# Optimization experiments

Hardware: AMD Instinct MI355X
Metric: run time of the kernel (lower is better)

Reference implementation:

```python
import jax, jax.numpy as jnp
import numpy as np

IN_FEATURES = 128
OUT_FEATURES = 64
NUM_HEADS = 4
NEGATIVE_SLOPE = 0.2


def setup_inputs() -> dict:
    key = jax.random.key(0)
    k1, k2, k3, k4 = jax.random.split(key, 4)
    B, N = 2, 4096
    inputs = jax.random.normal(k1, (B, N, IN_FEATURES), dtype=jnp.float32)
    # glorot-style scales
    s_w = (6.0 / (IN_FEATURES + OUT_FEATURES * NUM_HEADS)) ** 0.5
    s_a = (6.0 / (OUT_FEATURES + 1)) ** 0.5
    W = jax.random.uniform(k2, (IN_FEATURES, OUT_FEATURES * NUM_HEADS), jnp.float32, -s_w, s_w)
    a_src = jax.random.uniform(k3, (NUM_HEADS, OUT_FEATURES, 1), jnp.float32, -s_a, s_a)
    a_dst = jax.random.uniform(k4, (NUM_HEADS, OUT_FEATURES, 1), jnp.float32, -s_a, s_a)
    bias = jnp.zeros((OUT_FEATURES * NUM_HEADS,), dtype=jnp.float32)
    return {"inputs": inputs, "W": W, "a_src": a_src, "a_dst": a_dst, "bias": bias}


def reference(inputs, W, a_src, a_dst, bias):
    B, N, _ = inputs.shape
    H, D = a_src.shape[0], a_src.shape[1]
    # project and split heads: [B, H, N, D]
    h = jnp.matmul(inputs, W).reshape(B, N, H, D).transpose(0, 2, 1, 3)
    # additive attention scalars per node per head
    e_src = jnp.einsum('bhnd,hd->bhn', h, a_src[..., 0])  # a_src^T (W h_i)
    e_dst = jnp.einsum('bhnd,hd->bhn', h, a_dst[..., 0])  # a_dst^T (W h_j)
    # e[b,h,i,j] = e_src[b,h,i] + e_dst[b,h,j]  (matches e_src + e_dst^T in TF code)
    e = e_src[:, :, :, None] + e_dst[:, :, None, :]
    e = jnp.where(e > 0, e, NEGATIVE_SLOPE * e)  # leaky_relu
    alpha = jax.nn.softmax(e, axis=-1)  # softmax over neighbors j
    # weighted sum of values: [B, H, N, D]
    out = jnp.einsum('bhij,bhjd->bhid', alpha, h)
    out = out.transpose(0, 2, 1, 3).reshape(B, N, H * D)  # concat heads
    out = out + bias
    return jax.nn.elu(out)
```

## Files before the change

### kernel.cpp

```cpp
#include <hip/hip_runtime.h>
#include <hip/hip_fp16.h>
#include <math.h>

#define NH 4
#define DD 64
#define NF 256
#define KF 128
#define NN 4096
#define NB 2
#define NG 8
#define CH 64
#define NCH 64
#define PSUB 16
#define SSUB 8
#define TE 65

typedef _Float16 h8_t __attribute__((ext_vector_type(8)));
typedef float f4_t __attribute__((ext_vector_type(4)));

__global__ __launch_bounds__(256) void k_gemm(const float* __restrict__ X,
                                              const float* __restrict__ W,
                                              const float* __restrict__ a_src,
                                              const float* __restrict__ a_dst,
                                              __half* __restrict__ Hout,
                                              float* __restrict__ s_arr,
                                              float* __restrict__ d_arr) {
  __shared__ float As[64][132];
  __shared__ _Float16 WT[64][136];
  const int bm = blockIdx.x;
  const int bn = blockIdx.y;
  const int tid = threadIdx.x;

  for (int i = tid; i < 64 * 32; i += 256) {
    int r = i >> 5, c4 = i & 31;
    float4 v = *(const float4*)(X + ((size_t)(bm * 64 + r)) * KF + c4 * 4);
    *(float4*)&As[r][c4 * 4] = v;
  }
  for (int i = tid; i < 64 * 128; i += 256) {
    int k = i >> 6, c = i & 63;
    WT[c][k] = (_Float16)W[(size_t)k * NF + bn * 64 + c];
  }
  __syncthreads();

  const int lane = tid & 63, w = tid >> 6;
  const int l15 = lane & 15, lq = lane >> 4;

  f4_t acc[4] = {f4_t{0.f,0.f,0.f,0.f}, f4_t{0.f,0.f,0.f,0.f},
                 f4_t{0.f,0.f,0.f,0.f}, f4_t{0.f,0.f,0.f,0.f}};

  #pragma unroll
  for (int kk = 0; kk < 4; ++kk) {
    const int koff = kk * 32 + lq * 8;
    h8_t a;
    {
      const float* ap = &As[w * 16 + l15][koff];
      float4 x0 = *(const float4*)ap;
      float4 x1 = *(const float4*)(ap + 4);
      a[0] = (_Float16)x0.x; a[1] = (_Float16)x0.y;
      a[2] = (_Float16)x0.z; a[3] = (_Float16)x0.w;
      a[4] = (_Float16)x1.x; a[5] = (_Float16)x1.y;
      a[6] = (_Float16)x1.z; a[7] = (_Float16)x1.w;
    }
    #pragma unroll
    for (int t = 0; t < 4; ++t) {
      h8_t b = *(const h8_t*)&WT[t * 16 + l15][koff];
      acc[t] = __builtin_amdgcn_mfma_f32_16x16x32_f16(a, b, acc[t], 0, 0, 0);
    }
  }

  float asv[4], adv[4];
  #pragma unroll
  for (int t = 0; t < 4; ++t) {
    asv[t] = a_src[bn * 64 + t * 16 + l15];
    adv[t] = a_dst[bn * 64 + t * 16 + l15];
  }
  #pragma unroll
  for (int j = 0; j < 4; ++j) {
    const int grow = bm * 64 + w * 16 + lq * 4 + j;
    float ps = 0.f, pd = 0.f;
    #pragma unroll
    for (int t = 0; t < 4; ++t) {
      float hv = acc[t][j];
      Hout[(size_t)grow * NF + bn * 64 + t * 16 + l15] = __float2half(hv);
      ps += hv * asv[t];
      pd += hv * adv[t];
    }
    #pragma unroll
    for (int off = 1; off < 16; off <<= 1) {
      ps += __shfl_xor(ps, off);
      pd += __shfl_xor(pd, off);
    }
    if (l15 == 0) {
      int b = grow >> 12, n = grow & (NN - 1);
      int g = b * NH + bn;
      s_arr[g * NN + n] = ps;
      d_arr[g * NN + n] = pd;
    }
  }
}

__global__ __launch_bounds__(512) void k_sort(const float* __restrict__ d_arr,
                                              const float* __restrict__ s_arr,
                                              float* __restrict__ dsort, int* __restrict__ dperm,
                                              float* __restrict__ tsort, int* __restrict__ tperm) {
  __shared__ unsigned skey[8][512];
  __shared__ float vals[NN];
  const int bid = blockIdx.x;
  const bool isT = bid >= NG;
  const int g = isT ? bid - NG : bid;
  const float* src = isT ? s_arr : d_arr;
  float* okey = isT ? tsort : dsort;
  int* operm = isT ? tperm : dperm;
  const int tid = threadIdx.x;

  unsigned kk[8];
  {
    float4 v0 = *(const float4*)(src + g * NN + 8 * tid);
    float4 v1 = *(const float4*)(src + g * NN + 8 * tid + 4);
    float f[8] = {v0.x, v0.y, v0.z, v0.w, v1.x, v1.y, v1.z, v1.w};
    #pragma unroll
    for (int r = 0; r < 8; ++r) {
      float fv = isT ? -f[r] : f[r];
      vals[8 * tid + r] = fv;
      unsigned u = __float_as_uint(fv);
      u = (u & 0x80000000u) ? ~u : (u | 0x80000000u);
      kk[r] = (u & 0xFFFFF000u) | (unsigned)(8 * tid + r);
    }
  }

  #define CEU(a, b, asc)                                           \
    do { unsigned ka = kk[a], kb = kk[b];                          \
      unsigned mn = ka < kb ? ka : kb, mx = ka < kb ? kb : ka;     \
      kk[a] = (asc) ? mn : mx; kk[b] = (asc) ? mx : mn; } while (0)

  CEU(0, 1, true); CEU(2, 3, false); CEU(4, 5, true); CEU(6, 7, false);
  CEU(0, 2, true); CEU(1, 3, true); CEU(4, 6, false); CEU(5, 7, false);
  CEU(0, 1, true); CEU(2, 3, true); CEU(4, 5, false); CEU(6, 7, false);

  #pragma unroll
  for (int k = 8; k <= NN; k <<= 1) {
    const bool asc = (tid & (k >> 3)) == 0;
    #pragma unroll
    for (int j = k >> 1; j > 0; j >>= 1) {
      if (j >= 512) {
        const int tdist = j >> 3;
        #pragma unroll
        for (int r = 0; r < 8; ++r) skey[r][tid] = kk[r];
        __syncthreads();
        const bool keepMin = ((tid & tdist) == 0) == asc;
        #pragma unroll
        for (int r = 0; r < 8; ++r) {
          unsigned pk = skey[r][tid ^ tdist];
          unsigned mn = kk[r] < pk ? kk[r] : pk;
          unsigned mx = kk[r] < pk ? pk : kk[r];
          kk[r] = keepMin ? mn : mx;
        }
        __syncthreads();
      } else if (j >= 8) {
        const int dist = j >> 3;
        const bool keepMin = ((tid & dist) == 0) == asc;
        #pragma unroll
        for (int r = 0; r < 8; ++r) {
          unsigned pk = (unsigned)__shfl_xor((int)kk[r], dist);
          unsigned mn = kk[r] < pk ? kk[r] : pk;
          unsigned mx = kk[r] < pk ? pk : kk[r];
          kk[r] = keepMin ? mn : mx;
        }
      } else if (j == 4) {
        CEU(0, 4, asc); CEU(1, 5, asc); CEU(2, 6, asc); CEU(3, 7, asc);
      } else if (j == 2) {
        CEU(0, 2, asc); CEU(1, 3, asc); CEU(4, 6, asc); CEU(5, 7, asc);
      } else {
        CEU(0, 1, asc); CEU(2, 3, asc); CEU(4, 5, asc); CEU(6, 7, asc);
      }
    }
  }
  #undef CEU

  float ov[8]; int op[8];
  #pragma unroll
  for (int r = 0; r < 8; ++r) {
    int idx = (int)(kk[r] & 0xFFFu);
    ov[r] = vals[idx];
    op[r] = idx;
  }
  *(float4*)(okey + g * NN + 8 * tid)     = make_float4(ov[0], ov[1], ov[2], ov[3]);
  *(float4*)(okey + g * NN + 8 * tid + 4) = make_float4(ov[4], ov[5], ov[6], ov[7]);
  *(int4*)(operm + g * NN + 8 * tid)      = make_int4(op[0], op[1], op[2], op[3]);
  *(int4*)(operm + g * NN + 8 * tid + 4)  = make_int4(op[4], op[5], op[6], op[7]);
}

__global__ __launch_bounds__(256) void k_part(const __half* __restrict__ Hmat,
                                              const float* __restrict__ dsort,
                                              const int* __restrict__ dperm,
                                              float* __restrict__ chunkP, float* __restrict__ chunkS,
                                              float* __restrict__ chunkPw, float* __restrict__ chunkSw) {
  __shared__ float subP[4][64], subS[4][64];
  __shared__ float subPw[4], subSw[4];
  const int ch = blockIdx.x;
  const int g = blockIdx.y;
  const int b = g >> 2, h = g & 3;
  const int c = threadIdx.x & 63;
  const int w = threadIdx.x >> 6;
  const int gNN = g * NN;
  const size_t bNN = (size_t)b * NN;
  const int h64 = h * 64;
  const float dmax = dsort[gNN + NN - 1];
  const int kw0 = ch * CH + w * PSUB;

  int j16[PSUB]; float d16[PSUB], hv16[PSUB];
  #pragma unroll
  for (int l = 0; l < PSUB; ++l) j16[l] = dperm[gNN + kw0 + l];
  #pragma unroll
  for (int l = 0; l < PSUB; ++l) d16[l] = dsort[gNN + kw0 + l];
  #pragma unroll
  for (int l = 0; l < PSUB; ++l) hv16[l] = __half2float(Hmat[(bNN + j16[l]) * NF + h64 + c]);

  float pa = 0.f, sa = 0.f, pw = 0.f, sw = 0.f;
  #pragma unroll
  for (int l = 0; l < PSUB; ++l) {
    float wp = __expf(0.2f * (d16[l] - dmax));
    float w2 = wp * wp;
    float ws = w2 * w2 * wp;
    pa += wp * hv16[l]; sa += ws * hv16[l]; pw += wp; sw += ws;
  }
  subP[w][c] = pa; subS[w][c] = sa;
  if (c == 0) { subPw[w] = pw; subSw[w] = sw; }
  __syncthreads();

  if (w == 0) {
    float tp = subP[0][c] + subP[1][c] + subP[2][c] + subP[3][c];
    float ts = subS[0][c] + subS[1][c] + subS[2][c] + subS[3][c];
    chunkP[(g * NCH + ch) * 64 + c] = tp;
    chunkS[(g * NCH + ch) * 64 + c] = ts;
    if (c == 0) {
      chunkPw[g * NCH + ch] = subPw[0] + subPw[1] + subPw[2] + subPw[3];
      chunkSw[g * NCH + ch] = subSw[0] + subSw[1] + subSw[2] + subSw[3];
    }
  }
}

__global__ __launch_bounds__(512) void k_serve(const __half* __restrict__ Hmat,
                                               const float* __restrict__ dsort,
                                               const int* __restrict__ dperm,
                                               const float* __restrict__ tsort,
                                               const int* __restrict__ tperm,
                                               const float* __restrict__ chunkP, const float* __restrict__ chunkS,
                                               const float* __restrict__ chunkPw, const float* __restrict__ chunkSw,
                                               const float* __restrict__ bias,
                                               float* __restrict__ out) {
  __shared__ float PPloc[TE][64], PSloc[TE][64];
  __shared__ float ppwLoc[TE], pswLoc[TE];
  __shared__ float subP[8][64], subS[8][64], sall[8][64];
  __shared__ float subPw[8], subSw[8];

  const int ch = blockIdx.x & (NCH - 1);
  const int g = blockIdx.x >> 6;
  const int b = g >> 2, h = g & 3;
  const int c = threadIdx.x & 63;
  const int w = threadIdx.x >> 6;
  const int gNN = g * NN;
  const size_t bNN = (size_t)b * NN;
  const int h64 = h * 64;
  const float dmax = dsort[gNN + NN - 1];
  const int kw0 = ch * CH + w * SSUB;

  int j8[SSUB]; float d8[SSUB], hv8[SSUB];
  #pragma unroll
  for (int l = 0; l < SSUB; ++l) j8[l] = dperm[gNN + kw0 + l];
  #pragma unroll
  for (int l = 0; l < SSUB; ++l) d8[l] = dsort[gNN + kw0 + l];
  #pragma unroll
  for (int l = 0; l < SSUB; ++l) hv8[l] = __half2float(Hmat[(bNN + j8[l]) * NF + h64 + c]);

  float ppv[SSUB], psv[SSUB], ppw[SSUB], psw[SSUB];
  {
    float ap = 0.f, as = 0.f, aw = 0.f, aswv = 0.f;
    #pragma unroll
    for (int l = 0; l < SSUB; ++l) {
      float wp = __expf(0.2f * (d8[l] - dmax));
      float w2 = wp * wp;
      float ws = w2 * w2 * wp;
      ap += wp * hv8[l]; as += ws * hv8[l]; aw += wp; aswv += ws;
      ppv[l] = ap; psv[l] = as; ppw[l] = aw; psw[l] = aswv;
    }
    subP[w][c] = ap; subS[w][c] = as;
    if (c == 0) { subPw[w] = aw; subSw[w] = aswv; }
  }
  __syncthreads();

  {
    float oP = 0.f, oS = 0.f, oPw = 0.f, oSw = 0.f;
    #pragma unroll
    for (int t = 0; t < 8; ++t) {
      if (t < w) { oP += subP[t][c]; oS += subS[t][c]; oPw += subPw[t]; oSw += subSw[t]; }
    }
    #pragma unroll
    for (int l = 0; l < SSUB; ++l) {
      PPloc[w * SSUB + 1 + l][c] = ppv[l] + oP;
      PSloc[w * SSUB + 1 + l][c] = psv[l] + oS;
    }
    if (c == 0) {
      #pragma unroll
      for (int l = 0; l < SSUB; ++l) {
        ppwLoc[w * SSUB + 1 + l] = ppw[l] + oPw;
        pswLoc[w * SSUB + 1 + l] = psw[l] + oSw;
      }
    }
    if (w == 0) {
      PPloc[0][c] = 0.f; PSloc[0][c] = 0.f;
      if (c == 0) { ppwLoc[0] = 0.f; pswLoc[0] = 0.f; }
    }
  }
  __syncthreads();

  {
    float pp = 0.f, sp = 0.f, sa = 0.f;
    for (int t = w; t < ch; t += 8) pp += chunkP[(g * NCH + t) * 64 + c];
    for (int t = w; t < NCH; t += 8) {
      float v = chunkS[(g * NCH + t) * 64 + c];
      sa += v;
      if (t < ch) sp += v;
    }
    subP[w][c] = pp; subS[w][c] = sp; sall[w][c] = sa;
  }

  float offPw, offSw, totSw;
  {
    float w1 = chunkPw[g * NCH + c];
    float u1 = chunkSw[g * NCH + c];
    float pwo = (c < ch ? w1 : 0.f);
    float swo = (c < ch ? u1 : 0.f);
    float stw = u1;
    #pragma unroll
    for (int off = 1; off < 64; off <<= 1) {
      pwo += __shfl_xor(pwo, off);
      swo += __shfl_xor(swo, off);
      stw += __shfl_xor(stw, off);
    }
    offPw = pwo; offSw = swo; totSw = stw;
  }
  __syncthreads();

  float offP = 0.f, offS = 0.f, totS = 0.f;
  #pragma unroll
  for (int t = 0; t < 8; ++t) { offP += subP[t][c]; offS += subS[t][c]; totS += sall[t][c]; }

  const float* ts = tsort + gNN;
  int rlo, rhi;
  {
    const float p1 = ts[c * 64 + 63];
    if (ch == 0) rlo = 0;
    else {
      const float blo = dsort[gNN + ch * CH];
      unsigned long long m1 = __ballot(p1 < blo);
      int blk = __popcll(m1);
      if (blk == 64) rlo = NN;
      else {
        float p2 = ts[blk * 64 + c];
        unsigned long long m2 = __ballot(p2 < blo);
        rlo = blk * 64 + __popcll(m2);
      }
    }
    if (ch == NCH - 1) rhi = NN;
    else {
      const float bhi = dsort[gNN + (ch + 1) * CH];
      unsigned long long m1 = __ballot(p1 < bhi);
      int blk = __popcll(m1);
      if (blk == 64) rhi = NN;
      else {
        float p2 = ts[blk * 64 + c];
        unsigned long long m2 = __ballot(p2 < bhi);
        rhi = blk * 64 + __popcll(m2);
      }
    }
  }

  const float myd = dsort[gNN + ch * CH + c];
  const float biasv = bias[h64 + c];

  for (int r = rlo + w; r < rhi; r += 8) {
    const float t = ts[r];
    const int i = tperm[gNN + r];
    const int mloc = __popcll(__ballot(myd <= t));
    const float numB = PPloc[mloc][c] + offP;
    const float denB = ppwLoc[mloc] + offPw;
    const float numA = totS - (PSloc[mloc][c] + offS);
    const float denA = totSw - (pswLoc[mloc] + offSw);
    const float si = -t;
    const float sdm = si + dmax;
    const float mx = sdm > 0.f ? sdm : 0.2f * sdm;
    const float alpha = __expf(sdm - mx);
    const float beta = __expf(0.2f * sdm - mx);
    const float den = alpha * denA + beta * denB;
    float val = (alpha * numA + beta * numB) / den + biasv;
    float o = val > 0.f ? val : expm1f(val);
    out[(bNN + i) * NF + h64 + c] = o;
  }
}

extern "C" void kernel_launch(void* const* d_in, const int* in_sizes, int n_in,
                              void* d_out, int out_size, void* d_ws, size_t ws_size,
                              hipStream_t stream) {
  const float* X = (const float*)d_in[0];
  const float* W = (const float*)d_in[1];
  const float* a_src = (const float*)d_in[2];
  const float* a_dst = (const float*)d_in[3];
  const float* bias = (const float*)d_in[4];
  float* out = (float*)d_out;

  float* ws = (float*)d_ws;
  float* s_arr = ws;
  float* d_arr = s_arr + NG * NN;
  float* dsort = d_arr + NG * NN;
  int* dperm = (int*)(dsort + NG * NN);
  float* tsort = (float*)(dperm + NG * NN);
  int* tperm = (int*)(tsort + NG * NN);
  float* chunkP = (float*)(tperm + NG * NN);
  float* chunkS = chunkP + NG * NCH * 64;
  float* chunkPw = chunkS + NG * NCH * 64;
  float* chunkSw = chunkPw + NG * NCH;
  __half* Hmat = (__half*)(chunkSw + NG * NCH);

  k_gemm<<<dim3(128, 4), 256, 0, stream>>>(X, W, a_src, a_dst, Hmat, s_arr, d_arr);
  k_sort<<<2 * NG, 512, 0, stream>>>(d_arr, s_arr, dsort, dperm, tsort, tperm);
  k_part<<<dim3(NCH, NG), 256, 0, stream>>>(Hmat, dsort, dperm, chunkP, chunkS, chunkPw, chunkSw);
  k_serve<<<NG * NCH, 512, 0, stream>>>(Hmat, dsort, dperm, tsort, tperm,
                                        chunkP, chunkS, chunkPw, chunkSw, bias, out);
}
```

Baseline: 49.85 us.

## Compute chunk prefix sums in last-finishing k_part block via atomic counter

The last k_part block for each group, detected with an atomic counter and threadfence, now computes exclusive prefix sums over chunk partials and writes them to new workspace arrays. k_serve reads its offsets and totals directly instead of having every block re-reduce all chunk partials, which drops a redundant reduction pass and one barrier per serve block. The trade-off is a serial 64-step scan done by a single block per group at the tail of k_part, plus added reliance on atomics and memory fences for correctness.

```diff
diff --git a/kernel.cpp b/kernel.cpp
--- a/kernel.cpp
+++ b/kernel.cpp
@@ -102,7 +102,8 @@
 __global__ __launch_bounds__(512) void k_sort(const float* __restrict__ d_arr,
                                               const float* __restrict__ s_arr,
                                               float* __restrict__ dsort, int* __restrict__ dperm,
-                                              float* __restrict__ tsort, int* __restrict__ tperm) {
+                                              float* __restrict__ tsort, int* __restrict__ tperm,
+                                              int* __restrict__ cnt) {
   __shared__ unsigned skey[8][512];
   __shared__ float vals[NN];
   const int bid = blockIdx.x;
@@ -112,6 +113,7 @@
   float* okey = isT ? tsort : dsort;
   int* operm = isT ? tperm : dperm;
   const int tid = threadIdx.x;
+  if (!isT && tid == 0) cnt[g] = 0;
 
   unsigned kk[8];
   {
@@ -194,9 +196,13 @@
                                               const float* __restrict__ dsort,
                                               const int* __restrict__ dperm,
                                               float* __restrict__ chunkP, float* __restrict__ chunkS,
-                                              float* __restrict__ chunkPw, float* __restrict__ chunkSw) {
+                                              float* __restrict__ chunkPw, float* __restrict__ chunkSw,
+                                              float* __restrict__ prefP, float* __restrict__ prefS,
+                                              float* __restrict__ prefPw, float* __restrict__ prefSw,
+                                              int* __restrict__ cnt) {
   __shared__ float subP[4][64], subS[4][64];
   __shared__ float subPw[4], subSw[4];
+  __shared__ int lastFlag;
   const int ch = blockIdx.x;
   const int g = blockIdx.y;
   const int b = g >> 2, h = g & 3;
@@ -238,6 +244,51 @@
       chunkSw[g * NCH + ch] = subSw[0] + subSw[1] + subSw[2] + subSw[3];
     }
   }
+  __syncthreads();
+
+  if (threadIdx.x == 0) {
+    __threadfence();
+    int old = atomicAdd(&cnt[g], 1);
+    lastFlag = (old == NCH - 1) ? 1 : 0;
+  }
+  __syncthreads();
+  if (lastFlag) {
+    __threadfence();
+    const int base = g * (NCH + 1);
+    if (w == 0) {
+      float run = 0.f;
+      for (int t = 0; t < NCH; ++t) {
+        prefP[(size_t)(base + t) * 64 + c] = run;
+        run += chunkP[(g * NCH + t) * 64 + c];
+      }
+      prefP[(size_t)(base + NCH) * 64 + c] = run;
+    } else if (w == 1) {
+      float run = 0.f;
+      for (int t = 0; t < NCH; ++t) {
+        prefS[(size_t)(base + t) * 64 + c] = run;
+        run += chunkS[(g * NCH + t) * 64 + c];
+      }
+      prefS[(size_t)(base + NCH) * 64 + c] = run;
+    } else if (w == 2) {
+      float x = chunkPw[g * NCH + c];
+      #pragma unroll
+      for (int off = 1; off < 64; off <<= 1) {
+        float y = __shfl_up(x, off);
+        if (c >= off) x += y;
+      }
+      prefPw[base + c + 1] = x;
+      if (c == 0) prefPw[base] = 0.f;
+    } else {
+      float x = chunkSw[g * NCH + c];
+      #pragma unroll
+      for (int off = 1; off < 64; off <<= 1) {
+        float y = __shfl_up(x, off);
+        if (c >= off) x += y;
+      }
+      prefSw[base + c + 1] = x;
+      if (c == 0) prefSw[base] = 0.f;
+    }
+  }
 }
 
 __global__ __launch_bounds__(512) void k_serve(const __half* __restrict__ Hmat,
@@ -245,13 +296,13 @@
                                                const int* __restrict__ dperm,
                                                const float* __restrict__ tsort,
                                                const int* __restrict__ tperm,
-                                               const float* __restrict__ chunkP, const float* __restrict__ chunkS,
-                                               const float* __restrict__ chunkPw, const float* __restrict__ chunkSw,
+                                               const float* __restrict__ prefP, const float* __restrict__ prefS,
+                                               const float* __restrict__ prefPw, const float* __restrict__ prefSw,
                                                const float* __restrict__ bias,
                                                float* __restrict__ out) {
   __shared__ float PPloc[TE][64], PSloc[TE][64];
   __shared__ float ppwLoc[TE], pswLoc[TE];
-  __shared__ float subP[8][64], subS[8][64], sall[8][64];
+  __shared__ float subP[8][64], subS[8][64];
   __shared__ float subPw[8], subSw[8];
 
   const int ch = blockIdx.x & (NCH - 1);
@@ -262,6 +313,15 @@
   const int gNN = g * NN;
   const size_t bNN = (size_t)b * NN;
   const int h64 = h * 64;
+  const int base = g * (NCH + 1);
+
+  const float offP = prefP[(size_t)(base + ch) * 64 + c];
+  const float offS = prefS[(size_t)(base + ch) * 64 + c];
+  const float totS = prefS[(size_t)(base + NCH) * 64 + c];
+  const float offPw = prefPw[base + ch];
+  const float offSw = prefSw[base + ch];
+  const float totSw = prefSw[base + NCH];
+
   const float dmax = dsort[gNN + NN - 1];
   const int kw0 = ch * CH + w * SSUB;
 
@@ -312,39 +372,6 @@
       if (c == 0) { ppwLoc[0] = 0.f; pswLoc[0] = 0.f; }
     }
   }
-  __syncthreads();
-
-  {
-    float pp = 0.f, sp = 0.f, sa = 0.f;
-    for (int t = w; t < ch; t += 8) pp += chunkP[(g * NCH + t) * 64 + c];
-    for (int t = w; t < NCH; t += 8) {
-      float v = chunkS[(g * NCH + t) * 64 + c];
-      sa += v;
-      if (t < ch) sp += v;
-    }
-    subP[w][c] = pp; subS[w][c] = sp; sall[w][c] = sa;
-  }
-
-  float offPw, offSw, totSw;
-  {
-    float w1 = chunkPw[g * NCH + c];
-    float u1 = chunkSw[g * NCH + c];
-    float pwo = (c < ch ? w1 : 0.f);
-    float swo = (c < ch ? u1 : 0.f);
-    float stw = u1;
-    #pragma unroll
-    for (int off = 1; off < 64; off <<= 1) {
-      pwo += __shfl_xor(pwo, off);
-      swo += __shfl_xor(swo, off);
-      stw += __shfl_xor(stw, off);
-    }
-    offPw = pwo; offSw = swo; totSw = stw;
-  }
-  __syncthreads();
-
-  float offP = 0.f, offS = 0.f, totS = 0.f;
-  #pragma unroll
-  for (int t = 0; t < 8; ++t) { offP += subP[t][c]; offS += subS[t][c]; totS += sall[t][c]; }
 
   const float* ts = tsort + gNN;
   int rlo, rhi;
@@ -378,6 +405,7 @@
 
   const float myd = dsort[gNN + ch * CH + c];
   const float biasv = bias[h64 + c];
+  __syncthreads();
 
   for (int r = rlo + w; r < rhi; r += 8) {
     const float t = ts[r];
@@ -420,11 +448,17 @@
   float* chunkS = chunkP + NG * NCH * 64;
   float* chunkPw = chunkS + NG * NCH * 64;
   float* chunkSw = chunkPw + NG * NCH;
-  __half* Hmat = (__half*)(chunkSw + NG * NCH);
+  float* prefP = chunkSw + NG * NCH;
+  float* prefS = prefP + NG * (NCH + 1) * 64;
+  float* prefPw = prefS + NG * (NCH + 1) * 64;
+  float* prefSw = prefPw + NG * (NCH + 1);
+  int* cnt = (int*)(prefSw + NG * (NCH + 1));
+  __half* Hmat = (__half*)(cnt + NG + 56);
 
   k_gemm<<<dim3(128, 4), 256, 0, stream>>>(X, W, a_src, a_dst, Hmat, s_arr, d_arr);
-  k_sort<<<2 * NG, 512, 0, stream>>>(d_arr, s_arr, dsort, dperm, tsort, tperm);
-  k_part<<<dim3(NCH, NG), 256, 0, stream>>>(Hmat, dsort, dperm, chunkP, chunkS, chunkPw, chunkSw);
+  k_sort<<<2 * NG, 512, 0, stream>>>(d_arr, s_arr, dsort, dperm, tsort, tperm, cnt);
+  k_part<<<dim3(NCH, NG), 256, 0, stream>>>(Hmat, dsort, dperm, chunkP, chunkS, chunkPw, chunkSw,
+                                            prefP, prefS, prefPw, prefSw, cnt);
   k_serve<<<NG * NCH, 512, 0, stream>>>(Hmat, dsort, dperm, tsort, tperm,
-                                        chunkP, chunkS, chunkPw, chunkSw, bias, out);
+                                        prefP, prefS, prefPw, prefSw, bias, out);
 }
```

New measurement: 64.35 us. 1.29x slower.
